# Kernel tuning notes

Hardware: AMD Instinct MI355X
Metric: run time of the kernel (lower is better)

## Reference

```python
import jax, jax.numpy as jnp
import numpy as np

SCALE_DTYPE = jnp.float32

def rotate_half(x):
    half = x.shape[-1] // 2
    return jnp.concatenate([-x[..., half:], x[..., :half]], axis=-1)

def apply_rope(x, cos, sin):
    # x: [B,T,H,Dh]; cos/sin: [T,Dh] -> broadcast to [1,T,1,Dh]
    c = cos[None, :, None, :]
    s = sin[None, :, None, :]
    return x * c + rotate_half(x) * s

def setup_inputs() -> dict:
    key = jax.random.key(0)
    ks = jax.random.split(key, 7)
    B, T, D, H, Dh = 4, 2048, 1024, 16, 64
    x = jax.random.normal(ks[0], (B, T, D), dtype=jnp.float32)
    cos = jax.random.uniform(ks[1], (T, Dh), dtype=jnp.float32)
    sin = jax.random.uniform(ks[2], (T, Dh), dtype=jnp.float32)
    scale = 1.0 / np.sqrt(D)
    Wq = jax.random.normal(ks[3], (D, D), dtype=jnp.float32) * scale
    Wk = jax.random.normal(ks[4], (D, D), dtype=jnp.float32) * scale
    Wv = jax.random.normal(ks[5], (D, D), dtype=jnp.float32) * scale
    Wo = jax.random.normal(ks[6], (D, D), dtype=jnp.float32) * scale
    return {"x": x, "cos": cos, "sin": sin, "Wq": Wq, "Wk": Wk, "Wv": Wv, "Wo": Wo}

def reference(x, cos, sin, Wq, Wk, Wv, Wo):
    B, T, D = x.shape
    H, Dh = 16, 64
    # Linear projections (weights stored [in, out]) and split heads
    q = (x @ Wq).reshape(B, T, H, Dh)
    k = (x @ Wk).reshape(B, T, H, Dh)
    v = (x @ Wv).reshape(B, T, H, Dh)
    q = apply_rope(q, cos[:T], sin[:T])
    k = apply_rope(k, cos[:T], sin[:T])
    scale = 1.0 / jnp.sqrt(jnp.asarray(Dh, dtype=x.dtype))
    # [B,H,T,T] causal scores
    scores = jnp.einsum('bthd,bshd->bhts', q, k) * scale
    causal = jnp.tril(jnp.ones((T, T), dtype=bool))
    scores = jnp.where(causal[None, None, :, :], scores, jnp.asarray(-jnp.inf, dtype=scores.dtype))
    weights = jax.nn.softmax(scores, axis=-1)
    out = jnp.einsum('bhts,bshd->bthd', weights, v).reshape(B, T, D)
    return out @ Wo
```

## Files before the change

### kernel.cpp

```cpp
#include <hip/hip_runtime.h>
#include <cstdint>
#include <cstddef>

typedef unsigned short ushort_t;
typedef __attribute__((ext_vector_type(8))) short short8;
typedef __attribute__((ext_vector_type(4))) float float4v;
typedef __attribute__((ext_vector_type(4))) unsigned short ushort4v;

__device__ __forceinline__ float b2f(ushort_t u) {
    uint32_t x = ((uint32_t)u) << 16;
    float f;
    __builtin_memcpy(&f, &x, 4);
    return f;
}
__device__ __forceinline__ ushort_t f2b(float f) {
    uint32_t x;
    __builtin_memcpy(&x, &f, 4);
    uint32_t r = (x + 0x7fffu + ((x >> 16) & 1u)) >> 16;
    return (ushort_t)r;
}
__device__ __forceinline__ ushort_t f2b_trunc(float f) {
    uint32_t x;
    __builtin_memcpy(&x, &f, 4);
    return (ushort_t)(x >> 16);
}

typedef __attribute__((address_space(3))) void lds_void;
typedef __attribute__((address_space(1))) const void gbl_void;
__device__ __forceinline__ void gload16(const void* g, void* l) {
    __builtin_amdgcn_global_load_lds((gbl_void*)(uintptr_t)g, (lds_void*)(uintptr_t)l, 16, 0, 0);
}

__global__ void detect_dtype(const ushort_t* __restrict__ cosp, int* __restrict__ flag) {
    int tid = threadIdx.x;
    int bad = 0;
    for (int i = tid; i < 512; i += 64) {
        ushort_t u = cosp[i];
        int sign = u >> 15;
        int e = (u >> 7) & 0xFF;
        if (sign || e > 126) bad = 1;
    }
    int anybad = __any(bad);
    if (tid == 0) *flag = anybad ? 1 : 0;
}

__global__ __launch_bounds__(256) void prep_all(const void* __restrict__ x,
                                                ushort_t* __restrict__ xb,
                                                const void* __restrict__ c,
                                                const void* __restrict__ s,
                                                ushort_t* __restrict__ cb,
                                                ushort_t* __restrict__ sb,
                                                const void* __restrict__ w0,
                                                const void* __restrict__ w1,
                                                const void* __restrict__ w2,
                                                const void* __restrict__ w3,
                                                ushort_t* __restrict__ wt,
                                                const int* __restrict__ flag) {
    __shared__ ushort_t tile[32][33];
    int z = blockIdx.z;
    int f = *flag;
    if (z < 4) {
        const void* in = (z == 0) ? w0 : (z == 1) ? w1 : (z == 2) ? w2 : w3;
        ushort_t* o = wt + (size_t)z * 1024 * 1024;
        int bx = blockIdx.x * 32;
        int by = blockIdx.y * 32;
        int tx = threadIdx.x & 31;
        int ty = threadIdx.x >> 5;
        for (int r = ty; r < 32; r += 8) {
            size_t idx = (size_t)(by + r) * 1024 + bx + tx;
            tile[r][tx] = f ? f2b(((const float*)in)[idx]) : ((const ushort_t*)in)[idx];
        }
        __syncthreads();
        for (int r = ty; r < 32; r += 8)
            o[(size_t)(bx + r) * 1024 + by + tx] = tile[tx][r];
    } else if (z == 4) {
        int i = (blockIdx.y * 32 + blockIdx.x) * 256 + threadIdx.x;
        if (i < 131072) {
            if (f) {
                cb[i] = f2b(((const float*)c)[i]);
                sb[i] = f2b(((const float*)s)[i]);
            } else {
                cb[i] = ((const ushort_t*)c)[i];
                sb[i] = ((const ushort_t*)s)[i];
            }
        }
    } else {
        if (f == 0) return;
        int bid = (z - 5) * 1024 + blockIdx.y * 32 + blockIdx.x;
        int i = (bid * 256 + threadIdx.x) * 4;
        float4v v = *(const float4v*)((const float*)x + i);
        ushort4v o4;
#pragma unroll
        for (int j = 0; j < 4; ++j) o4[j] = f2b(v[j]);
        *(ushort4v*)(xb + i) = o4;
    }
}

template <int W>
__device__ __forceinline__ void vm_wait() {
    if constexpr (W == 6)      asm volatile("s_waitcnt vmcnt(6)" ::: "memory");
    else                       asm volatile("s_waitcnt vmcnt(0)" ::: "memory");
}
#define KBAR()                                       \
    do {                                             \
        asm volatile("" ::: "memory");               \
        __builtin_amdgcn_s_barrier();                \
        asm volatile("" ::: "memory");               \
    } while (0)

__global__ __launch_bounds__(512, 2) void gemm_qkv(const ushort_t* __restrict__ X0,
                                                   const ushort_t* __restrict__ X1,
                                                   const ushort_t* __restrict__ Wt,
                                                   ushort_t* __restrict__ qk,
                                                   ushort_t* __restrict__ vt,
                                                   const ushort_t* __restrict__ cosb,
                                                   const ushort_t* __restrict__ sinb,
                                                   const int* __restrict__ flagp) {
    __shared__ ushort_t LDS[73728];
    char* LDSc = (char*)LDS;

    int tid = threadIdx.x;
    int lane = tid & 63;
    int wave = tid >> 6;
    int wm = wave >> 1;
    int wn = wave & 1;
    int quad = lane >> 4;
    int l16 = lane & 15;

    int id = blockIdx.x;
    int xcd = id & 7;
    int r = id >> 3;
    int m0 = (xcd * 4 + (r & 3)) * 256;
    int n0 = (r >> 2) * 128;

    const ushort_t* Xb = (*flagp) ? X1 : X0;

    int lrow = lane >> 3;
    int lslot = (lane & 7) ^ lrow;
    const ushort_t* aSrc = Xb + (size_t)(m0 + wave * 32 + lrow) * 1024 + lslot * 8;
    const ushort_t* bSrc = Wt + (size_t)(n0 + wave * 16 + lrow) * 1024 + lslot * 8;
    int ldsA_w = (wave * 32) * 128;
    int ldsB_w = (wave * 16) * 128;

    int aoff0 = (wm * 64 + l16) * 128 + ((quad ^ (l16 & 7)) * 16);
    int aoff1 = (wm * 64 + l16) * 128 + (((4 + quad) ^ (l16 & 7)) * 16);
    int boff0 = (wn * 64 + l16) * 128 + ((quad ^ (l16 & 7)) * 16);
    int boff1 = (wn * 64 + l16) * 128 + (((4 + quad) ^ (l16 & 7)) * 16);

    float4v acc[4][4];
#pragma unroll
    for (int i = 0; i < 4; ++i)
#pragma unroll
        for (int n = 0; n < 4; ++n) acc[i][n] = (float4v){0.f, 0.f, 0.f, 0.f};

#define STAGE6(t, jj)                                                       \
    do {                                                                    \
        const ushort_t* as_ = aSrc + (jj) * 64;                             \
        const ushort_t* bs_ = bSrc + (jj) * 64;                             \
        char* al_ = LDSc + (t) * 32768 + ldsA_w;                            \
        char* bl_ = LDSc + 98304 + (t) * 16384 + ldsB_w;                    \
        gload16(as_, al_);                                                  \
        gload16(as_ + 8 * 1024, al_ + 1024);                                \
        gload16(as_ + 16 * 1024, al_ + 2048);                               \
        gload16(as_ + 24 * 1024, al_ + 3072);                               \
        gload16(bs_, bl_);                                                  \
        gload16(bs_ + 8 * 1024, bl_ + 1024);                                \
    } while (0)

#define COMPUTE(t)                                                          \
    do {                                                                    \
        const char* ab_ = LDSc + (t) * 32768;                               \
        const char* bb_ = LDSc + 98304 + (t) * 16384;                       \
        short8 a0_[4], b0_[4], a1_[4], b1_[4];                              \
        _Pragma("unroll") for (int i = 0; i < 4; ++i) {                     \
            a0_[i] = *(const short8*)(ab_ + aoff0 + i * 2048);              \
            a1_[i] = *(const short8*)(ab_ + aoff1 + i * 2048);              \
        }                                                                   \
        _Pragma("unroll") for (int n = 0; n < 4; ++n) {                     \
            b0_[n] = *(const short8*)(bb_ + boff0 + n * 2048);              \
            b1_[n] = *(const short8*)(bb_ + boff1 + n * 2048);              \
        }                                                                   \
        __builtin_amdgcn_s_setprio(1);                                      \
        _Pragma("unroll") for (int i = 0; i < 4; ++i)                       \
            _Pragma("unroll") for (int n = 0; n < 4; ++n)                   \
                acc[i][n] = __builtin_amdgcn_mfma_f32_16x16x32_bf16(        \
                    a0_[i], b0_[n], acc[i][n], 0, 0, 0);                    \
        _Pragma("unroll") for (int i = 0; i < 4; ++i)                       \
            _Pragma("unroll") for (int n = 0; n < 4; ++n)                   \
                acc[i][n] = __builtin_amdgcn_mfma_f32_16x16x32_bf16(        \
                    a1_[i], b1_[n], acc[i][n], 0, 0, 0);                    \
        __builtin_amdgcn_s_setprio(0);                                      \
    } while (0)

    STAGE6(0, 0);
    STAGE6(1, 1);
    vm_wait<6>();
    KBAR();

#pragma unroll 1
    for (int g = 0; g < 4; ++g) {
        int j = g * 3;
        STAGE6(2, j + 2);
        COMPUTE(0);
        vm_wait<6>();
        KBAR();
        STAGE6(0, j + 3);
        COMPUTE(1);
        vm_wait<6>();
        KBAR();
        STAGE6(1, j + 4);
        COMPUTE(2);
        vm_wait<6>();
        KBAR();
    }
    STAGE6(2, 14);
    COMPUTE(0);
    vm_wait<6>();
    KBAR();
    STAGE6(0, 15);
    COMPUTE(1);
    vm_wait<6>();
    KBAR();
    COMPUTE(2);
    vm_wait<0>();
    KBAR();
    COMPUTE(0);

#undef STAGE6
#undef COMPUTE

    int nglob = n0 + wn * 64;
    int region = nglob >> 10;
    int hcol = (nglob & 1023) >> 6;

    if (region < 2) {
        float scl = (region == 0) ? 0.18033688f : 1.0f;
        int colbase = region * 1024 + hcol * 64 + l16;
#pragma unroll
        for (int i = 0; i < 4; ++i) {
            int rowb = m0 + wm * 64 + i * 16 + quad * 4;
#pragma unroll
            for (int rr = 0; rr < 4; ++rr) {
                int row = rowb + rr;
                int t = row & 2047;
                const ushort_t* cp = cosb + t * 64 + l16;
                const ushort_t* sp = sinb + t * 64 + l16;
                float c0 = b2f(cp[0]), c1 = b2f(cp[16]), c2 = b2f(cp[32]), c3 = b2f(cp[48]);
                float s0v = b2f(sp[0]), s1v = b2f(sp[16]), s2v = b2f(sp[32]), s3v = b2f(sp[48]);
                float a0 = acc[i][0][rr], a1 = acc[i][1][rr], a2 = acc[i][2][rr], a3 = acc[i][3][rr];
                float o0 = (a0 * c0 - a2 * s0v) * scl;
                float o1 = (a1 * c1 - a3 * s1v) * scl;
                float o2 = (a2 * c2 + a0 * s2v) * scl;
                float o3 = (a3 * c3 + a1 * s3v) * scl;
                size_t base = (size_t)row * 2048 + colbase;
                qk[base] = f2b(o0);
                qk[base + 16] = f2b(o1);
                qk[base + 32] = f2b(o2);
                qk[base + 48] = f2b(o3);
            }
        }
    } else {
#pragma unroll
        for (int i = 0; i < 4; ++i) {
            int rowb = m0 + wm * 64 + i * 16 + quad * 4;
            int b = rowb >> 11;
            int t0 = rowb & 2047;
            size_t hb = (size_t)(b * 16 + hcol) * 64;
#pragma unroll
            for (int n = 0; n < 4; ++n) {
                int d = l16 + n * 16;
                ushort4v pk;
#pragma unroll
                for (int rr = 0; rr < 4; ++rr) pk[rr] = f2b(acc[i][n][rr]);
                *(ushort4v*)(vt + (hb + d) * 2048 + t0) = pk;
            }
        }
    }
}

__global__ __launch_bounds__(512, 2) void gemm_proj(const ushort_t* __restrict__ A, int lda,
                                                    const ushort_t* __restrict__ Bt,
                                                    void* __restrict__ C, int ldc,
                                                    int K,
                                                    const int* __restrict__ flagp) {
    __shared__ ushort_t LDS[73728];
    char* LDSc = (char*)LDS;

    int tid = threadIdx.x;
    int lane = tid & 63;
    int wave = tid >> 6;
    int wm = wave >> 1;
    int wn = wave & 1;
    int quad = lane >> 4;
    int l16 = lane & 15;

    int id = blockIdx.x;
    int xcd = id & 7;
    int r = id >> 3;
    int m0 = (xcd * 4 + (r & 3)) * 256;
    int n0 = (r >> 2) * 128;

    int lrow = lane >> 3;
    int lslot = (lane & 7) ^ lrow;
    const ushort_t* aSrc = A + (size_t)(m0 + wave * 32 + lrow) * lda + lslot * 8;
    const ushort_t* bSrc = Bt + (size_t)(n0 + wave * 16 + lrow) * K + lslot * 8;
    int ldsA_w = (wave * 32) * 128;
    int ldsB_w = (wave * 16) * 128;
    int astr = 8 * lda;
    int bstr = 8 * K;

    int aoff0 = (wm * 64 + l16) * 128 + ((quad ^ (l16 & 7)) * 16);
    int aoff1 = (wm * 64 + l16) * 128 + (((4 + quad) ^ (l16 & 7)) * 16);
    int boff0 = (wn * 64 + l16) * 128 + ((quad ^ (l16 & 7)) * 16);
    int boff1 = (wn * 64 + l16) * 128 + (((4 + quad) ^ (l16 & 7)) * 16);

    float4v acc[4][4];
#pragma unroll
    for (int i = 0; i < 4; ++i)
#pragma unroll
        for (int n = 0; n < 4; ++n) acc[i][n] = (float4v){0.f, 0.f, 0.f, 0.f};

#define STAGE6P(t, jj)                                                      \
    do {                                                                    \
        const ushort_t* as_ = aSrc + (jj) * 64;                             \
        const ushort_t* bs_ = bSrc + (jj) * 64;                             \
        char* al_ = LDSc + (t) * 32768 + ldsA_w;                            \
        char* bl_ = LDSc + 98304 + (t) * 16384 + ldsB_w;                    \
        gload16(as_, al_);                                                  \
        gload16(as_ + astr, al_ + 1024);                                    \
        gload16(as_ + 2 * astr, al_ + 2048);                                \
        gload16(as_ + 3 * astr, al_ + 3072);                                \
        gload16(bs_, bl_);                                                  \
        gload16(bs_ + bstr, bl_ + 1024);                                    \
    } while (0)

#define COMPUTEP(t)                                                         \
    do {                                                                    \
        const char* ab_ = LDSc + (t) * 32768;                               \
        const char* bb_ = LDSc + 98304 + (t) * 16384;                       \
        short8 a0_[4], b0_[4], a1_[4], b1_[4];                              \
        _Pragma("unroll") for (int i = 0; i < 4; ++i) {                     \
            a0_[i] = *(const short8*)(ab_ + aoff0 + i * 2048);              \
            a1_[i] = *(const short8*)(ab_ + aoff1 + i * 2048);              \
        }                                                                   \
        _Pragma("unroll") for (int n = 0; n < 4; ++n) {                     \
            b0_[n] = *(const short8*)(bb_ + boff0 + n * 2048);              \
            b1_[n] = *(const short8*)(bb_ + boff1 + n * 2048);              \
        }                                                                   \
        __builtin_amdgcn_s_setprio(1);                                      \
        _Pragma("unroll") for (int i = 0; i < 4; ++i)                       \
            _Pragma("unroll") for (int n = 0; n < 4; ++n)                   \
                acc[i][n] = __builtin_amdgcn_mfma_f32_16x16x32_bf16(        \
                    a0_[i], b0_[n], acc[i][n], 0, 0, 0);                    \
        _Pragma("unroll") for (int i = 0; i < 4; ++i)                       \
            _Pragma("unroll") for (int n = 0; n < 4; ++n)                   \
                acc[i][n] = __builtin_amdgcn_mfma_f32_16x16x32_bf16(        \
                    a1_[i], b1_[n], acc[i][n], 0, 0, 0);                    \
        __builtin_amdgcn_s_setprio(0);                                      \
    } while (0)

    STAGE6P(0, 0);
    STAGE6P(1, 1);
    vm_wait<6>();
    KBAR();

#pragma unroll 1
    for (int g = 0; g < 4; ++g) {
        int j = g * 3;
        STAGE6P(2, j + 2);
        COMPUTEP(0);
        vm_wait<6>();
        KBAR();
        STAGE6P(0, j + 3);
        COMPUTEP(1);
        vm_wait<6>();
        KBAR();
        STAGE6P(1, j + 4);
        COMPUTEP(2);
        vm_wait<6>();
        KBAR();
    }
    STAGE6P(2, 14);
    COMPUTEP(0);
    vm_wait<6>();
    KBAR();
    STAGE6P(0, 15);
    COMPUTEP(1);
    vm_wait<6>();
    KBAR();
    COMPUTEP(2);
    vm_wait<0>();
    KBAR();
    COMPUTEP(0);

#undef STAGE6P
#undef COMPUTEP

    int f32out = *flagp;
#pragma unroll
    for (int i = 0; i < 4; ++i) {
        int rowb = m0 + wm * 64 + i * 16 + quad * 4;
#pragma unroll
        for (int rr = 0; rr < 4; ++rr) {
            size_t base = (size_t)(rowb + rr) * ldc + n0 + wn * 64 + l16;
            if (f32out) {
                float* Cf = (float*)C;
#pragma unroll
                for (int n = 0; n < 4; ++n) Cf[base + n * 16] = acc[i][n][rr];
            } else {
                ushort_t* Cb = (ushort_t*)C;
#pragma unroll
                for (int n = 0; n < 4; ++n) Cb[base + n * 16] = f2b(acc[i][n][rr]);
            }
        }
    }
}

__global__ __launch_bounds__(512, 4) void attn_mfma(ushort_t* qk,
                                                    const ushort_t* __restrict__ vt) {
    __shared__ ushort_t Kl[2][4096];
    __shared__ ushort_t Vl[2][4096];
    __shared__ ushort_t Pl[8 * 16 * 72];

    int tid = threadIdx.x;
    int lane = tid & 63;
    int wave = tid >> 6;
    int quad = lane >> 4;
    int l16 = lane & 15;

    int id = blockIdx.x;
    int bxi = (id >> 3) & 7;
    int bh = (id & 7) * 8 + (id >> 6);
    int b = bh >> 4;
    int h = bh & 15;

    ushort_t* Pw = &Pl[wave * 16 * 72];

    int rr = tid >> 3;
    int sl = (tid & 7) ^ (rr & 7);
    const ushort_t* ksrc = qk + (size_t)(b * 2048 + rr) * 2048 + 1024 + h * 64 + sl * 8;
    const ushort_t* vsrc = vt + (size_t)(bh * 64 + rr) * 2048 + sl * 8;
    char* kdst = (char*)&Kl[0][0] + wave * 1024;
    char* vdst = (char*)&Vl[0][0] + wave * 1024;

    int swr = l16 & 7;

#pragma unroll 1
    for (int phase = 0; phase < 2; ++phase) {
        int qt = phase ? bxi : (15 - bxi);
        int row0 = qt * 128 + wave * 16;
        size_t qbase = ((size_t)(b * 2048 + row0)) * 2048 + h * 64;

        short8 qf[2];
        {
            const ushort_t* p = qk + qbase + (size_t)l16 * 2048 + quad * 8;
            qf[0] = *(const short8*)p;
            qf[1] = *(const short8*)(p + 32);
        }

        float4v oacc[4];
#pragma unroll
        for (int nt = 0; nt < 4; ++nt) oacc[nt] = (float4v){0.f, 0.f, 0.f, 0.f};
        float psum[4];
#pragma unroll
        for (int r = 0; r < 4; ++r) psum[r] = 0.f;

        int ntiles = 2 * qt + 2;

        gload16(ksrc, kdst);
        gload16(vsrc, vdst);
        vm_wait<0>();
        KBAR();

        for (int st = 0; st < ntiles; ++st) {
            int s0 = st * 64;
            int buf = st & 1;

            if (st + 1 < ntiles) {
                gload16(ksrc + (size_t)(s0 + 64) * 2048, kdst + ((st + 1) & 1) * 8192);
                gload16(vsrc + (s0 + 64), vdst + ((st + 1) & 1) * 8192);
            }

            if (s0 <= row0 + 15) {
                const char* kb = (const char*)&Kl[buf][0];
                const char* vb = (const char*)&Vl[buf][0];

                float4v sacc[4];
#pragma unroll
                for (int ct = 0; ct < 4; ++ct) sacc[ct] = (float4v){0.f, 0.f, 0.f, 0.f};
#pragma unroll
                for (int ks = 0; ks < 2; ++ks) {
                    short8 bfr[4];
#pragma unroll
                    for (int ct = 0; ct < 4; ++ct)
                        bfr[ct] = *(const short8*)(kb + (ct * 16 + l16) * 128 +
                                                   (((ks * 4 + quad) ^ swr) * 16));
                    __builtin_amdgcn_s_setprio(1);
#pragma unroll
                    for (int ct = 0; ct < 4; ++ct)
                        sacc[ct] = __builtin_amdgcn_mfma_f32_16x16x32_bf16(
                            qf[ks], bfr[ct], sacc[ct], 0, 0, 0);
                    __builtin_amdgcn_s_setprio(0);
                }

                if ((s0 + 63) > row0) {
#pragma unroll
                    for (int r = 0; r < 4; ++r) {
                        int trow = row0 + quad * 4 + r;
                        float ps = 0.f;
#pragma unroll
                        for (int ct = 0; ct < 4; ++ct) {
                            float p = exp2f(sacc[ct][r]);
                            if ((s0 + ct * 16 + l16) > trow) p = 0.f;
                            ps += p;
                            Pw[(quad * 4 + r) * 72 + ct * 16 + l16] = f2b_trunc(p);
                        }
                        psum[r] += ps;
                    }
                } else {
#pragma unroll
                    for (int r = 0; r < 4; ++r) {
                        float ps = 0.f;
#pragma unroll
                        for (int ct = 0; ct < 4; ++ct) {
                            float p = exp2f(sacc[ct][r]);
                            ps += p;
                            Pw[(quad * 4 + r) * 72 + ct * 16 + l16] = f2b_trunc(p);
                        }
                        psum[r] += ps;
                    }
                }

#pragma unroll
                for (int ks = 0; ks < 2; ++ks) {
                    short8 bfr[4];
#pragma unroll
                    for (int nt = 0; nt < 4; ++nt)
                        bfr[nt] = *(const short8*)(vb + (nt * 16 + l16) * 128 +
                                                   (((ks * 4 + quad) ^ swr) * 16));
                    short8 af = *(const short8*)(&Pw[l16 * 72 + ks * 32 + quad * 8]);
                    __builtin_amdgcn_s_setprio(1);
#pragma unroll
                    for (int nt = 0; nt < 4; ++nt)
                        oacc[nt] = __builtin_amdgcn_mfma_f32_16x16x32_bf16(
                            af, bfr[nt], oacc[nt], 0, 0, 0);
                    __builtin_amdgcn_s_setprio(0);
                }
            }

            vm_wait<0>();
            KBAR();
        }

#pragma unroll
        for (int r = 0; r < 4; ++r) {
            float ps = psum[r];
#pragma unroll
            for (int off = 1; off < 16; off <<= 1) ps += __shfl_xor(ps, off);
            float inv = 1.0f / ps;
            size_t base = qbase + (size_t)(quad * 4 + r) * 2048;
#pragma unroll
            for (int nt = 0; nt < 4; ++nt)
                qk[base + nt * 16 + l16] = f2b(oacc[nt][r] * inv);
        }
    }
}

extern "C" void kernel_launch(void* const* d_in, const int* in_sizes, int n_in,
                              void* d_out, int out_size, void* d_ws, size_t ws_size,
                              hipStream_t stream) {
    const void* x = d_in[0];
    const void* cosp = d_in[1];
    const void* sinp = d_in[2];
    const void* Wq = d_in[3];
    const void* Wk = d_in[4];
    const void* Wv = d_in[5];
    const void* Wo = d_in[6];

    char* ws = (char*)d_ws;
    int* flag = (int*)ws;
    ushort_t* vtg = (ushort_t*)(ws + 256);
    ushort_t* qk = vtg + (size_t)8192 * 2048;
    ushort_t* WT = qk + (size_t)8192 * 2048;
    ushort_t* WoT = WT + (size_t)3 * 1024 * 1024;
    ushort_t* cosb = WT + (size_t)4 * 1024 * 1024;
    ushort_t* sinb = cosb + (size_t)2048 * 64;
    ushort_t* xb = sinb + (size_t)2048 * 64;

    detect_dtype<<<1, 64, 0, stream>>>((const ushort_t*)cosp, flag);
    prep_all<<<dim3(32, 32, 13), 256, 0, stream>>>(x, xb, cosp, sinp, cosb, sinb,
                                                   Wq, Wk, Wv, Wo, WT, flag);

    gemm_qkv<<<768, 512, 0, stream>>>((const ushort_t*)x, xb, WT, qk, vtg, cosb, sinb, flag);

    attn_mfma<<<512, 512, 0, stream>>>(qk, vtg);

    gemm_proj<<<256, 512, 0, stream>>>(qk, 2048, WoT, d_out, 1024, 1024, flag);
}
```

Baseline: 241.5 us.

## Enlarge QKV GEMM tile to 256x256 with split-K half-stage pipeline

The QKV projection GEMM moves from 256x128 to 256x256 output tiles, with an 8x4 accumulator grid per wave and half the number of blocks. The K loop is restructured into half-K slots that are double-buffered, interleaving loads with four MFMA phases separated by barriers. The goal is higher operand reuse per LDS byte and fewer global loads per FLOP. The costs are more accumulator registers, which could lower occupancy or cause spills, many extra barriers, and only 384 blocks to fill the GPU.

```diff
diff --git a/kernel.cpp b/kernel.cpp
--- a/kernel.cpp
+++ b/kernel.cpp
@@ -98,8 +98,10 @@
 
 template <int W>
 __device__ __forceinline__ void vm_wait() {
-    if constexpr (W == 6)      asm volatile("s_waitcnt vmcnt(6)" ::: "memory");
-    else                       asm volatile("s_waitcnt vmcnt(0)" ::: "memory");
+    if constexpr (W == 8)      asm volatile("s_waitcnt vmcnt(8)" ::: "memory");
+    else if constexpr (W == 6) asm volatile("s_waitcnt vmcnt(6)" ::: "memory");
+    else if constexpr (W == 4) asm volatile("s_waitcnt vmcnt(4)" ::: "memory");
+    else if constexpr (W == 0) asm volatile("s_waitcnt vmcnt(0)" ::: "memory");
 }
 #define KBAR()                                       \
     do {                                             \
@@ -116,14 +118,14 @@
                                                    const ushort_t* __restrict__ cosb,
                                                    const ushort_t* __restrict__ sinb,
                                                    const int* __restrict__ flagp) {
-    __shared__ ushort_t LDS[73728];
+    __shared__ ushort_t LDS[65536];
     char* LDSc = (char*)LDS;
 
     int tid = threadIdx.x;
     int lane = tid & 63;
     int wave = tid >> 6;
-    int wm = wave >> 1;
-    int wn = wave & 1;
+    int wm = wave >> 2;
+    int wn = wave & 3;
     int quad = lane >> 4;
     int l16 = lane & 15;
 
@@ -131,103 +133,106 @@
     int xcd = id & 7;
     int r = id >> 3;
     int m0 = (xcd * 4 + (r & 3)) * 256;
-    int n0 = (r >> 2) * 128;
+    int n0 = (r >> 2) * 256;
 
     const ushort_t* Xb = (*flagp) ? X1 : X0;
 
-    int lrow = lane >> 3;
-    int lslot = (lane & 7) ^ lrow;
-    const ushort_t* aSrc = Xb + (size_t)(m0 + wave * 32 + lrow) * 1024 + lslot * 8;
-    const ushort_t* bSrc = Wt + (size_t)(n0 + wave * 16 + lrow) * 1024 + lslot * 8;
-    int ldsA_w = (wave * 32) * 128;
-    int ldsB_w = (wave * 16) * 128;
-
-    int aoff0 = (wm * 64 + l16) * 128 + ((quad ^ (l16 & 7)) * 16);
-    int aoff1 = (wm * 64 + l16) * 128 + (((4 + quad) ^ (l16 & 7)) * 16);
-    int boff0 = (wn * 64 + l16) * 128 + ((quad ^ (l16 & 7)) * 16);
-    int boff1 = (wn * 64 + l16) * 128 + (((4 + quad) ^ (l16 & 7)) * 16);
-
-    float4v acc[4][4];
-#pragma unroll
-    for (int i = 0; i < 4; ++i)
+    const ushort_t* aS = Xb + (size_t)(m0 + wave * 32 + (lane >> 2)) * 1024 +
+                         (((lane & 3) ^ ((lane >> 2) & 3)) * 8);
+    const ushort_t* bS = Wt + (size_t)(n0 + wave * 32 + (lane >> 2)) * 1024 +
+                         (((lane & 3) ^ ((lane >> 2) & 3)) * 8);
+
+    int aoff = (wm * 128 + l16) * 64 + ((quad ^ (l16 & 3)) * 16);
+    int boff = (wn * 64 + l16) * 64 + ((quad ^ (l16 & 3)) * 16);
+
+    float4v acc[8][4];
+#pragma unroll
+    for (int i = 0; i < 8; ++i)
 #pragma unroll
         for (int n = 0; n < 4; ++n) acc[i][n] = (float4v){0.f, 0.f, 0.f, 0.f};
 
-#define STAGE6(t, jj)                                                       \
-    do {                                                                    \
-        const ushort_t* as_ = aSrc + (jj) * 64;                             \
-        const ushort_t* bs_ = bSrc + (jj) * 64;                             \
-        char* al_ = LDSc + (t) * 32768 + ldsA_w;                            \
-        char* bl_ = LDSc + 98304 + (t) * 16384 + ldsB_w;                    \
-        gload16(as_, al_);                                                  \
-        gload16(as_ + 8 * 1024, al_ + 1024);                                \
-        gload16(as_ + 16 * 1024, al_ + 2048);                               \
-        gload16(as_ + 24 * 1024, al_ + 3072);                               \
-        gload16(bs_, bl_);                                                  \
-        gload16(bs_ + 8 * 1024, bl_ + 1024);                                \
+#define SLOTB(BF, KH, ISB) (((((BF)*2 + (KH)) * 2) + (ISB)) * 16384)
+#define STAGE_A(BF, KH, JJ)                                                  \
+    do {                                                                     \
+        const ushort_t* s_ = aS + (JJ) * 64 + (KH) * 32;                     \
+        char* d_ = LDSc + SLOTB(BF, KH, 0) + wave * 2048;                    \
+        gload16(s_, d_);                                                     \
+        gload16(s_ + 16 * 1024, d_ + 1024);                                  \
     } while (0)
-
-#define COMPUTE(t)                                                          \
-    do {                                                                    \
-        const char* ab_ = LDSc + (t) * 32768;                               \
-        const char* bb_ = LDSc + 98304 + (t) * 16384;                       \
-        short8 a0_[4], b0_[4], a1_[4], b1_[4];                              \
-        _Pragma("unroll") for (int i = 0; i < 4; ++i) {                     \
-            a0_[i] = *(const short8*)(ab_ + aoff0 + i * 2048);              \
-            a1_[i] = *(const short8*)(ab_ + aoff1 + i * 2048);              \
-        }                                                                   \
-        _Pragma("unroll") for (int n = 0; n < 4; ++n) {                     \
-            b0_[n] = *(const short8*)(bb_ + boff0 + n * 2048);              \
-            b1_[n] = *(const short8*)(bb_ + boff1 + n * 2048);              \
-        }                                                                   \
-        __builtin_amdgcn_s_setprio(1);                                      \
-        _Pragma("unroll") for (int i = 0; i < 4; ++i)                       \
-            _Pragma("unroll") for (int n = 0; n < 4; ++n)                   \
-                acc[i][n] = __builtin_amdgcn_mfma_f32_16x16x32_bf16(        \
-                    a0_[i], b0_[n], acc[i][n], 0, 0, 0);                    \
-        _Pragma("unroll") for (int i = 0; i < 4; ++i)                       \
-            _Pragma("unroll") for (int n = 0; n < 4; ++n)                   \
-                acc[i][n] = __builtin_amdgcn_mfma_f32_16x16x32_bf16(        \
-                    a1_[i], b1_[n], acc[i][n], 0, 0, 0);                    \
-        __builtin_amdgcn_s_setprio(0);                                      \
+#define STAGE_B(BF, KH, JJ)                                                  \
+    do {                                                                     \
+        const ushort_t* s_ = bS + (JJ) * 64 + (KH) * 32;                     \
+        char* d_ = LDSc + SLOTB(BF, KH, 1) + wave * 2048;                    \
+        gload16(s_, d_);                                                     \
+        gload16(s_ + 16 * 1024, d_ + 1024);                                  \
     } while (0)
 
-    STAGE6(0, 0);
-    STAGE6(1, 1);
-    vm_wait<6>();
+#define PHASEMFMA(MG)                                                        \
+    do {                                                                     \
+        __builtin_amdgcn_s_barrier();                                        \
+        asm volatile("s_waitcnt lgkmcnt(0)" ::: "memory");                   \
+        __builtin_amdgcn_s_setprio(1);                                       \
+        _Pragma("unroll") for (int i = 0; i < 4; ++i)                        \
+            _Pragma("unroll") for (int nt = 0; nt < 4; ++nt)                 \
+                acc[(MG)*4 + i][nt] = __builtin_amdgcn_mfma_f32_16x16x32_bf16( \
+                    afr[i], bfr[nt], acc[(MG)*4 + i][nt], 0, 0, 0);          \
+        __builtin_amdgcn_s_setprio(0);                                       \
+        __builtin_amdgcn_s_barrier();                                        \
+    } while (0)
+
+#define KTILE(C, J, VW2, VW4, S12, S34)                                          \
+    do {                                                                         \
+        short8 bfr[4], afr[4];                                                   \
+                                                         \
+        _Pragma("unroll") for (int nt = 0; nt < 4; ++nt)                         \
+            bfr[nt] = *(const short8*)(LDSc + SLOTB(C, 0, 1) + boff + nt * 1024);\
+        _Pragma("unroll") for (int i = 0; i < 4; ++i)                            \
+            afr[i] = *(const short8*)(LDSc + SLOTB(C, 0, 0) + aoff + i * 1024);  \
+        if (S12) STAGE_A(1 - (C), 1, (J) + 1);                                   \
+        PHASEMFMA(0);                                                            \
+                                                         \
+        _Pragma("unroll") for (int i = 0; i < 4; ++i)                            \
+            afr[i] = *(const short8*)(LDSc + SLOTB(C, 0, 0) + aoff + (4 + i) * 1024); \
+        if (S12) STAGE_B(1 - (C), 1, (J) + 1);                                   \
+        vm_wait<VW2>();                                                          \
+        PHASEMFMA(1);                                                            \
+                                                         \
+        _Pragma("unroll") for (int nt = 0; nt < 4; ++nt)                         \
+            bfr[nt] = *(const short8*)(LDSc + SLOTB(C, 1, 1) + boff + nt * 1024);\
+        _Pragma("unroll") for (int i = 0; i < 4; ++i)                            \
+            afr[i] = *(const short8*)(LDSc + SLOTB(C, 1, 0) + aoff + i * 1024);  \
+        if (S34) STAGE_A((C), 0, (J) + 2);                                       \
+        PHASEMFMA(0);                                                            \
+                                                         \
+        _Pragma("unroll") for (int i = 0; i < 4; ++i)                            \
+            afr[i] = *(const short8*)(LDSc + SLOTB(C, 1, 0) + aoff + (4 + i) * 1024); \
+        if (S34) STAGE_B((C), 0, (J) + 2);                                       \
+        vm_wait<VW4>();                                                          \
+        PHASEMFMA(1);                                                            \
+    } while (0)
+
+    STAGE_A(0, 0, 0);
+    STAGE_B(0, 0, 0);
+    STAGE_A(0, 1, 0);
+    STAGE_B(0, 1, 0);
+    STAGE_A(1, 0, 1);
+    STAGE_B(1, 0, 1);
+    vm_wait<8>();
     KBAR();
 
 #pragma unroll 1
-    for (int g = 0; g < 4; ++g) {
-        int j = g * 3;
-        STAGE6(2, j + 2);
-        COMPUTE(0);
-        vm_wait<6>();
-        KBAR();
-        STAGE6(0, j + 3);
-        COMPUTE(1);
-        vm_wait<6>();
-        KBAR();
-        STAGE6(1, j + 4);
-        COMPUTE(2);
-        vm_wait<6>();
-        KBAR();
+    for (int j = 0; j < 14; ++j) {
+        int c = j & 1;
+        KTILE(c, j, 8, 8, 1, 1);
     }
-    STAGE6(2, 14);
-    COMPUTE(0);
-    vm_wait<6>();
-    KBAR();
-    STAGE6(0, 15);
-    COMPUTE(1);
-    vm_wait<6>();
-    KBAR();
-    COMPUTE(2);
-    vm_wait<0>();
-    KBAR();
-    COMPUTE(0);
-
-#undef STAGE6
-#undef COMPUTE
+    KTILE(0, 14, 8, 4, 1, 0);
+    KTILE(1, 15, 0, -1, 0, 0);
+
+#undef KTILE
+#undef PHASEMFMA
+#undef STAGE_A
+#undef STAGE_B
+#undef SLOTB
 
     int nglob = n0 + wn * 64;
     int region = nglob >> 10;
@@ -237,8 +242,8 @@
         float scl = (region == 0) ? 0.18033688f : 1.0f;
         int colbase = region * 1024 + hcol * 64 + l16;
 #pragma unroll
-        for (int i = 0; i < 4; ++i) {
-            int rowb = m0 + wm * 64 + i * 16 + quad * 4;
+        for (int i = 0; i < 8; ++i) {
+            int rowb = m0 + wm * 128 + i * 16 + quad * 4;
 #pragma unroll
             for (int rr = 0; rr < 4; ++rr) {
                 int row = rowb + rr;
@@ -261,17 +266,17 @@
         }
     } else {
 #pragma unroll
-        for (int i = 0; i < 4; ++i) {
-            int rowb = m0 + wm * 64 + i * 16 + quad * 4;
+        for (int i = 0; i < 8; ++i) {
+            int rowb = m0 + wm * 128 + i * 16 + quad * 4;
             int b = rowb >> 11;
             int t0 = rowb & 2047;
             size_t hb = (size_t)(b * 16 + hcol) * 64;
 #pragma unroll
-            for (int n = 0; n < 4; ++n) {
-                int d = l16 + n * 16;
+            for (int nt = 0; nt < 4; ++nt) {
+                int d = l16 + nt * 16;
                 ushort4v pk;
 #pragma unroll
-                for (int rr = 0; rr < 4; ++rr) pk[rr] = f2b(acc[i][n][rr]);
+                for (int rr = 0; rr < 4; ++rr) pk[rr] = f2b(acc[i][nt][rr]);
                 *(ushort4v*)(vt + (hb + d) * 2048 + t0) = pk;
             }
         }
@@ -591,7 +596,7 @@
     prep_all<<<dim3(32, 32, 13), 256, 0, stream>>>(x, xb, cosp, sinp, cosb, sinb,
                                                    Wq, Wk, Wv, Wo, WT, flag);
 
-    gemm_qkv<<<768, 512, 0, stream>>>((const ushort_t*)x, xb, WT, qk, vtg, cosb, sinb, flag);
+    gemm_qkv<<<384, 512, 0, stream>>>((const ushort_t*)x, xb, WT, qk, vtg, cosb, sinb, flag);
 
     attn_mfma<<<512, 512, 0, stream>>>(qk, vtg);
 
```

New measurement: 262.3 us. 8.6% more time.
